# Kernel optimization log

Hardware: AMD Instinct MI355X
Metric: run time of the kernel (lower is better)

## Reference

```python
import jax, jax.numpy as jnp
import numpy as np

N_NODES = 100000


def setup_inputs() -> dict:
    key = jax.random.key(0)
    k1, k2, k3, k4 = jax.random.split(key, 4)
    E = 1600000
    D_IN, D_OUT = 256, 256
    feat = jax.random.normal(k1, (N_NODES, D_IN), dtype=jnp.float32)
    src = jax.random.randint(k2, (E,), 0, N_NODES, dtype=jnp.int32)
    dst = jax.random.randint(k3, (E,), 0, N_NODES, dtype=jnp.int32)
    # xavier_uniform-like init for weight
    limit = np.sqrt(6.0 / (D_IN + D_OUT)).astype(np.float32)
    weight = jax.random.uniform(k4, (D_IN, D_OUT), dtype=jnp.float32,
                                minval=-limit, maxval=limit)
    bias = jnp.zeros((D_OUT,), dtype=jnp.float32)
    return {"feat": feat, "src": src, "dst": dst, "weight": weight, "bias": bias}


def reference(feat, src, dst, weight, bias):
    ones = jnp.ones(src.shape[0], dtype=feat.dtype)
    # out_degrees: number of outgoing edges per node (src counts)
    out_deg = jax.ops.segment_sum(ones, src, num_segments=N_NODES)
    # in_degrees: number of incoming edges per node (dst counts)
    in_deg = jax.ops.segment_sum(ones, dst, num_segments=N_NODES)
    # norm == 'both': pre-scale by out_deg^-0.5
    pre = jnp.power(jnp.clip(out_deg, 1.0), -0.5)[:, None]  # [N,1]
    h = feat * pre
    # message passing: copy_src + sum over incoming edges (SpMM)
    agg = jax.ops.segment_sum(h[src], dst, num_segments=N_NODES)  # [N, D_in]
    # dense projection
    rst = agg @ weight  # [N, D_out]
    # post-scale by in_deg^-0.5
    post = jnp.power(jnp.clip(in_deg, 1.0), -0.5)[:, None]
    rst = rst * post + bias
    return rst
```

## Files before the change

### kernel.cpp

```cpp
#include <hip/hip_runtime.h>
#include <hip/hip_bf16.h>
#include <stdint.h>


using short8  = __attribute__((ext_vector_type(8))) short;
using floatx4 = __attribute__((ext_vector_type(4))) float;
using floatx2 = __attribute__((ext_vector_type(2))) float;
using ushort8 = __attribute__((ext_vector_type(8))) unsigned short;

static __device__ __forceinline__ unsigned short f32_to_bf16(float f) {
    unsigned int u = __float_as_uint(f);
    u += 0x7FFFu + ((u >> 16) & 1u);
    return (unsigned short)(u >> 16);
}
static __device__ __forceinline__ float bf2f(unsigned short u) {
    return __uint_as_float((unsigned int)u << 16);
}

__global__ void k_deg(const int* __restrict__ src, const int* __restrict__ dst,
                      int E, int* __restrict__ outc, int* __restrict__ inc) {
    int i = blockIdx.x * blockDim.x + threadIdx.x;
    int b = i * 4;
    if (b + 3 < E) {
        int4 s = *(const int4*)(src + b);
        int4 d = *(const int4*)(dst + b);
        atomicAdd(&outc[s.x], 1);
        atomicAdd(&outc[s.y], 1);
        atomicAdd(&outc[s.z], 1);
        atomicAdd(&outc[s.w], 1);
        atomicAdd(&inc[d.x], 1);
        atomicAdd(&inc[d.y], 1);
        atomicAdd(&inc[d.z], 1);
        atomicAdd(&inc[d.w], 1);
    } else {
        for (int j = b; j < E; ++j) {
            atomicAdd(&outc[src[j]], 1);
            atomicAdd(&inc[dst[j]], 1);
        }
    }
}

__global__ void k_off(const int* __restrict__ inc, int N, int* __restrict__ total,
                      int* __restrict__ cursor) {
    __shared__ int ss[256];
    __shared__ int sbase;
    int t = threadIdx.x;
    int i = blockIdx.x * 256 + t;
    int d = (i < N) ? inc[i] : 0;
    int v = d;
    ss[t] = v;
    __syncthreads();
    for (int off = 1; off < 256; off <<= 1) {
        int u = (t >= off) ? ss[t - off] : 0;
        __syncthreads();
        v += u;
        ss[t] = v;
        __syncthreads();
    }
    if (t == 255) sbase = atomicAdd(total, v);
    __syncthreads();
    if (i < N) cursor[i] = sbase + (v - d);
}

__global__ void k_fill(const int* __restrict__ src, const int* __restrict__ dst,
                       int E, int* __restrict__ cursor, int* __restrict__ eidx) {
    int i = blockIdx.x * blockDim.x + threadIdx.x;
    int b = i * 4;
    if (b + 3 < E) {
        int4 s = *(const int4*)(src + b);
        int4 d = *(const int4*)(dst + b);
        int p0 = atomicAdd(&cursor[d.x], 1);
        int p1 = atomicAdd(&cursor[d.y], 1);
        int p2 = atomicAdd(&cursor[d.z], 1);
        int p3 = atomicAdd(&cursor[d.w], 1);
        eidx[p0] = s.x;
        eidx[p1] = s.y;
        eidx[p2] = s.z;
        eidx[p3] = s.w;
    } else {
        for (int j = b; j < E; ++j) {
            int p = atomicAdd(&cursor[dst[j]], 1);
            eidx[p] = src[j];
        }
    }
}

__global__ void k_wt(const float* __restrict__ W, unsigned short* __restrict__ WT) {
    int i = blockIdx.x * blockDim.x + threadIdx.x;
    int n = i >> 8, k = i & 255;
    WT[n * 256 + k] = f32_to_bf16(W[(size_t)k * 256 + n]);
}

__global__ void __launch_bounds__(512, 4)
k_gemm(const float* __restrict__ feat, const int* __restrict__ outc,
       const unsigned short* __restrict__ WT, int N,
       unsigned short* __restrict__ z) {
    __shared__ unsigned short ldsB[256 * 128];

    int tid  = threadIdx.x;
    int wave = tid >> 6;
    int lane = tid & 63;
    int rl   = lane & 15;
    int g    = lane >> 4;
    int wm0  = blockIdx.x * 128 + wave * 16;
    int rowc = min(wm0 + rl, N - 1);
    float p  = rsqrtf((float)max(outc[rowc], 1));
    const floatx4* arow = (const floatx4*)(feat + (size_t)rowc * 256);
    int smask = (rl & 7) << 4;

    floatx4 acc[16];
#pragma unroll
    for (int n = 0; n < 16; ++n) acc[n] = (floatx4){0.f, 0.f, 0.f, 0.f};

#pragma unroll
    for (int h = 0; h < 2; ++h) {
        if (h) __syncthreads();
#pragma unroll
        for (int i = 0; i < 8; ++i) {
            int c    = i * 512 + tid;
            int r2   = c >> 4;
            int colb = (c & 15) << 4;
            ushort8 v = *(const ushort8*)(WT + r2 * 256 + h * 128 + (colb >> 1));
            int dst = r2 * 128 + ((colb ^ ((r2 & 7) << 4)) >> 1);
            *(ushort8*)(&ldsB[dst]) = v;
        }
        __syncthreads();

#pragma unroll
        for (int k2 = 0; k2 < 4; ++k2) {
            floatx4 v0 = __builtin_nontemporal_load(arow + h * 32 + k2 * 8 + g * 2);
            floatx4 v1 = __builtin_nontemporal_load(arow + h * 32 + k2 * 8 + g * 2 + 1);
            short8 a;
            a[0] = (short)f32_to_bf16(v0[0] * p);
            a[1] = (short)f32_to_bf16(v0[1] * p);
            a[2] = (short)f32_to_bf16(v0[2] * p);
            a[3] = (short)f32_to_bf16(v0[3] * p);
            a[4] = (short)f32_to_bf16(v1[0] * p);
            a[5] = (short)f32_to_bf16(v1[1] * p);
            a[6] = (short)f32_to_bf16(v1[2] * p);
            a[7] = (short)f32_to_bf16(v1[3] * p);
            int cb = (k2 * 64 + g * 16) ^ smask;
#pragma unroll
            for (int n = 0; n < 16; ++n) {
                short8 b = *(const short8*)(&ldsB[(n * 16 + rl) * 128 + (cb >> 1)]);
                acc[n] = __builtin_amdgcn_mfma_f32_16x16x32_bf16(a, b, acc[n], 0, 0, 0);
            }
        }
    }

#pragma unroll
    for (int n = 0; n < 16; ++n) {
        int c = n * 16 + rl;
#pragma unroll
        for (int i = 0; i < 4; ++i) {
            int rw = wm0 + g * 4 + i;
            if (rw < N) z[(size_t)rw * 256 + c] = f32_to_bf16(acc[n][i]);
        }
    }
}

__global__ void k_agg(const unsigned short* __restrict__ z,
                      const int* __restrict__ cursor, const int* __restrict__ inc,
                      const int* __restrict__ eidx, const float* __restrict__ bias,
                      int N, float* __restrict__ out) {
    int node = blockIdx.x * 4 + (threadIdx.x >> 6);
    if (node >= N) return;
    int h    = blockIdx.y;
    int lane = threadIdx.x & 63;
    int q    = lane >> 4;
    int sl   = lane & 15;
    int deg  = inc[node];
    const int* ep = eidx + (cursor[node] - deg);
    const unsigned short* zh = z + h * 128 + sl * 8;

    float accA[8], accB[8];
#pragma unroll
    for (int j = 0; j < 8; ++j) { accA[j] = 0.f; accB[j] = 0.f; }

    int e = 0;
    for (; e + 8 <= deg; e += 8) {
        int s0 = ep[e + q];
        int s1 = ep[e + 4 + q];
        ushort8 v0 = *(const ushort8*)(zh + (size_t)s0 * 256);
        ushort8 v1 = *(const ushort8*)(zh + (size_t)s1 * 256);
#pragma unroll
        for (int j = 0; j < 8; ++j) {
            accA[j] += bf2f(v0[j]);
            accB[j] += bf2f(v1[j]);
        }
    }
    for (; e < deg; e += 4) {
        if (e + q < deg) {
            int s = ep[e + q];
            ushort8 v = *(const ushort8*)(zh + (size_t)s * 256);
#pragma unroll
            for (int j = 0; j < 8; ++j) accA[j] += bf2f(v[j]);
        }
    }
#pragma unroll
    for (int j = 0; j < 8; ++j) accA[j] += accB[j];
#pragma unroll
    for (int j = 0; j < 8; ++j) accA[j] += __shfl_xor(accA[j], 16);
#pragma unroll
    for (int j = 0; j < 8; ++j) accA[j] += __shfl_xor(accA[j], 32);

    float post = rsqrtf((float)max(deg, 1));
    int c = h * 128 + sl * 8 + q * 2;
    floatx2 o;
    o[0] = accA[q * 2 + 0] * post + bias[c];
    o[1] = accA[q * 2 + 1] * post + bias[c + 1];
    __builtin_nontemporal_store(o, (floatx2*)(out + (size_t)node * 256 + c));
}

extern "C" void kernel_launch(void* const* d_in, const int* in_sizes, int n_in,
                              void* d_out, int out_size, void* d_ws, size_t ws_size,
                              hipStream_t stream) {
    const float* feat = (const float*)d_in[0];
    const int*   src  = (const int*)d_in[1];
    const int*   dst  = (const int*)d_in[2];
    const float* W    = (const float*)d_in[3];
    const float* bias = (const float*)d_in[4];
    float* out = (float*)d_out;

    const int D = 256;
    int N = in_sizes[0] / D;
    int E = in_sizes[1];

    char* ws = (char*)d_ws;
    size_t off = 0;
    auto alloc = [&](size_t bytes) -> void* {
        void* p = ws + off;
        off += (bytes + 255) & ~(size_t)255;
        return p;
    };
    int*            cnt    = (int*)alloc(((size_t)2 * N + 64) * sizeof(int));
    int*            outc   = cnt;
    int*            inc    = cnt + N;
    int*            total  = cnt + 2 * N;
    int*            cursor = (int*)alloc((size_t)N * sizeof(int));
    int*            eidx   = (int*)alloc((size_t)E * sizeof(int));
    unsigned short* z      = (unsigned short*)alloc((size_t)N * D * sizeof(unsigned short));
    unsigned short* WT     = (unsigned short*)alloc((size_t)D * D * sizeof(unsigned short));
    (void)ws_size;

    hipMemsetAsync(cnt, 0, ((size_t)2 * N + 64) * sizeof(int), stream);

    int tE4 = (E + 3) / 4;
    k_deg <<<(tE4 + 255) / 256, 256, 0, stream>>>(src, dst, E, outc, inc);
    k_off <<<(N + 255) / 256, 256, 0, stream>>>(inc, N, total, cursor);
    k_fill<<<(tE4 + 255) / 256, 256, 0, stream>>>(src, dst, E, cursor, eidx);
    k_wt  <<<(D * D) / 256, 256, 0, stream>>>(W, WT);
    k_gemm<<<(N + 127) / 128, 512, 0, stream>>>(feat, outc, WT, N, z);
    k_agg <<<dim3((N + 3) / 4, 2), 256, 0, stream>>>(z, cursor, inc, eidx, bias, N, out);
}
```

Before: 568.8 us.

## Merge CSR fill into GEMM launch so fill and projection overlap

The edge-fill (CSR build) kernel is folded into the GEMM kernel as extra leading blocks, so atomic scatter work and the MFMA projection can run concurrently in one launch. The GEMM's LDS tile of W is halved (64-wide K chunks over 4 passes) and the occupancy hint is dropped, which raises occupancy but adds more barriers. The degree and fill kernels also switch from int4 vector loads to coalesced scalar loads with two edges per thread.

```diff
diff --git a/kernel.cpp b/kernel.cpp
--- a/kernel.cpp
+++ b/kernel.cpp
@@ -19,24 +19,18 @@
 
 __global__ void k_deg(const int* __restrict__ src, const int* __restrict__ dst,
                       int E, int* __restrict__ outc, int* __restrict__ inc) {
-    int i = blockIdx.x * blockDim.x + threadIdx.x;
-    int b = i * 4;
-    if (b + 3 < E) {
-        int4 s = *(const int4*)(src + b);
-        int4 d = *(const int4*)(dst + b);
-        atomicAdd(&outc[s.x], 1);
-        atomicAdd(&outc[s.y], 1);
-        atomicAdd(&outc[s.z], 1);
-        atomicAdd(&outc[s.w], 1);
-        atomicAdd(&inc[d.x], 1);
-        atomicAdd(&inc[d.y], 1);
-        atomicAdd(&inc[d.z], 1);
-        atomicAdd(&inc[d.w], 1);
-    } else {
-        for (int j = b; j < E; ++j) {
-            atomicAdd(&outc[src[j]], 1);
-            atomicAdd(&inc[dst[j]], 1);
-        }
+    int base = blockIdx.x * 512;
+    int e0 = base + threadIdx.x;
+    int e1 = e0 + 256;
+    if (e0 < E) {
+        int s0 = src[e0], d0 = dst[e0];
+        atomicAdd(&outc[s0], 1);
+        atomicAdd(&inc[d0], 1);
+    }
+    if (e1 < E) {
+        int s1 = src[e1], d1 = dst[e1];
+        atomicAdd(&outc[s1], 1);
+        atomicAdd(&inc[d1], 1);
     }
 }
 
@@ -62,47 +56,45 @@
     if (i < N) cursor[i] = sbase + (v - d);
 }
 
-__global__ void k_fill(const int* __restrict__ src, const int* __restrict__ dst,
-                       int E, int* __restrict__ cursor, int* __restrict__ eidx) {
-    int i = blockIdx.x * blockDim.x + threadIdx.x;
-    int b = i * 4;
-    if (b + 3 < E) {
-        int4 s = *(const int4*)(src + b);
-        int4 d = *(const int4*)(dst + b);
-        int p0 = atomicAdd(&cursor[d.x], 1);
-        int p1 = atomicAdd(&cursor[d.y], 1);
-        int p2 = atomicAdd(&cursor[d.z], 1);
-        int p3 = atomicAdd(&cursor[d.w], 1);
-        eidx[p0] = s.x;
-        eidx[p1] = s.y;
-        eidx[p2] = s.z;
-        eidx[p3] = s.w;
-    } else {
-        for (int j = b; j < E; ++j) {
-            int p = atomicAdd(&cursor[dst[j]], 1);
-            eidx[p] = src[j];
-        }
-    }
-}
-
 __global__ void k_wt(const float* __restrict__ W, unsigned short* __restrict__ WT) {
     int i = blockIdx.x * blockDim.x + threadIdx.x;
     int n = i >> 8, k = i & 255;
     WT[n * 256 + k] = f32_to_bf16(W[(size_t)k * 256 + n]);
 }
 
-__global__ void __launch_bounds__(512, 4)
-k_gemm(const float* __restrict__ feat, const int* __restrict__ outc,
-       const unsigned short* __restrict__ WT, int N,
-       unsigned short* __restrict__ z) {
-    __shared__ unsigned short ldsB[256 * 128];
-
-    int tid  = threadIdx.x;
+__global__ void __launch_bounds__(512)
+k_fg(const int* __restrict__ src, const int* __restrict__ dst, int E,
+     int* __restrict__ cursor, int* __restrict__ eidx,
+     const float* __restrict__ feat, const int* __restrict__ outc,
+     const unsigned short* __restrict__ WT, int N, unsigned short* __restrict__ z,
+     int nbFill) {
+    __shared__ unsigned short ldsB[256 * 64];
+
+    int tid = threadIdx.x;
+
+    if ((int)blockIdx.x < nbFill) {
+        int base = blockIdx.x * 1024;
+        int e0 = base + tid;
+        int e1 = e0 + 512;
+        if (e0 < E) {
+            int s0 = src[e0];
+            int p0 = atomicAdd(&cursor[dst[e0]], 1);
+            eidx[p0] = s0;
+        }
+        if (e1 < E) {
+            int s1 = src[e1];
+            int p1 = atomicAdd(&cursor[dst[e1]], 1);
+            eidx[p1] = s1;
+        }
+        return;
+    }
+
+    int gbid = blockIdx.x - nbFill;
     int wave = tid >> 6;
     int lane = tid & 63;
     int rl   = lane & 15;
     int g    = lane >> 4;
-    int wm0  = blockIdx.x * 128 + wave * 16;
+    int wm0  = gbid * 128 + wave * 16;
     int rowc = min(wm0 + rl, N - 1);
     float p  = rsqrtf((float)max(outc[rowc], 1));
     const floatx4* arow = (const floatx4*)(feat + (size_t)rowc * 256);
@@ -113,23 +105,23 @@
     for (int n = 0; n < 16; ++n) acc[n] = (floatx4){0.f, 0.f, 0.f, 0.f};
 
 #pragma unroll
-    for (int h = 0; h < 2; ++h) {
+    for (int h = 0; h < 4; ++h) {
         if (h) __syncthreads();
 #pragma unroll
-        for (int i = 0; i < 8; ++i) {
+        for (int i = 0; i < 4; ++i) {
             int c    = i * 512 + tid;
-            int r2   = c >> 4;
-            int colb = (c & 15) << 4;
-            ushort8 v = *(const ushort8*)(WT + r2 * 256 + h * 128 + (colb >> 1));
-            int dst = r2 * 128 + ((colb ^ ((r2 & 7) << 4)) >> 1);
-            *(ushort8*)(&ldsB[dst]) = v;
+            int r2   = c >> 3;
+            int colb = (c & 7) << 4;
+            ushort8 v = *(const ushort8*)(WT + r2 * 256 + h * 64 + (colb >> 1));
+            int dstb = r2 * 64 + (((colb ^ ((r2 & 7) << 4))) >> 1);
+            *(ushort8*)(&ldsB[dstb]) = v;
         }
         __syncthreads();
 
 #pragma unroll
-        for (int k2 = 0; k2 < 4; ++k2) {
-            floatx4 v0 = __builtin_nontemporal_load(arow + h * 32 + k2 * 8 + g * 2);
-            floatx4 v1 = __builtin_nontemporal_load(arow + h * 32 + k2 * 8 + g * 2 + 1);
+        for (int kk = 0; kk < 2; ++kk) {
+            floatx4 v0 = __builtin_nontemporal_load(arow + h * 16 + kk * 8 + g * 2);
+            floatx4 v1 = __builtin_nontemporal_load(arow + h * 16 + kk * 8 + g * 2 + 1);
             short8 a;
             a[0] = (short)f32_to_bf16(v0[0] * p);
             a[1] = (short)f32_to_bf16(v0[1] * p);
@@ -139,10 +131,10 @@
             a[5] = (short)f32_to_bf16(v1[1] * p);
             a[6] = (short)f32_to_bf16(v1[2] * p);
             a[7] = (short)f32_to_bf16(v1[3] * p);
-            int cb = (k2 * 64 + g * 16) ^ smask;
+            int cb = (kk * 64 + g * 16) ^ smask;
 #pragma unroll
             for (int n = 0; n < 16; ++n) {
-                short8 b = *(const short8*)(&ldsB[(n * 16 + rl) * 128 + (cb >> 1)]);
+                short8 b = *(const short8*)(&ldsB[(n * 16 + rl) * 64 + (cb >> 1)]);
                 acc[n] = __builtin_amdgcn_mfma_f32_16x16x32_bf16(a, b, acc[n], 0, 0, 0);
             }
         }
@@ -245,11 +237,12 @@
 
     hipMemsetAsync(cnt, 0, ((size_t)2 * N + 64) * sizeof(int), stream);
 
-    int tE4 = (E + 3) / 4;
-    k_deg <<<(tE4 + 255) / 256, 256, 0, stream>>>(src, dst, E, outc, inc);
-    k_off <<<(N + 255) / 256, 256, 0, stream>>>(inc, N, total, cursor);
-    k_fill<<<(tE4 + 255) / 256, 256, 0, stream>>>(src, dst, E, cursor, eidx);
-    k_wt  <<<(D * D) / 256, 256, 0, stream>>>(W, WT);
-    k_gemm<<<(N + 127) / 128, 512, 0, stream>>>(feat, outc, WT, N, z);
-    k_agg <<<dim3((N + 3) / 4, 2), 256, 0, stream>>>(z, cursor, inc, eidx, bias, N, out);
-}
+    int nbFill = (E + 1023) / 1024;
+    int nbGemm = (N + 127) / 128;
+    k_deg<<<(E + 511) / 512, 256, 0, stream>>>(src, dst, E, outc, inc);
+    k_off<<<(N + 255) / 256, 256, 0, stream>>>(inc, N, total, cursor);
+    k_wt <<<(D * D) / 256, 256, 0, stream>>>(W, WT);
+    k_fg <<<nbFill + nbGemm, 512, 0, stream>>>(src, dst, E, cursor, eidx,
+                                               feat, outc, WT, N, z, nbFill);
+    k_agg<<<dim3((N + 3) / 4, 2), 256, 0, stream>>>(z, cursor, inc, eidx, bias, N, out);
+}
```

New measurement: 555.1 us. 2.4% less time.
